# Kernel tuning notes

Hardware: AMD Instinct MI355X
Metric: run time of the kernel (lower is better)

Reference implementation:

```python
import jax, jax.numpy as jnp
import numpy as np

N = 131072
MUL = 64  # multiplicity of each irrep in x
FAN_IN = 128  # 2*MUL input channels per output irrep block
INV_SQRT_FAN = float(1.0 / np.sqrt(FAN_IN))
INV_SQRT3 = float(1.0 / np.sqrt(3.0))


def setup_inputs() -> dict:
    key = jax.random.key(0)
    k1, k2, k3, k4 = jax.random.split(key, 4)
    x = jax.random.normal(k1, (N, MUL + MUL * 3), dtype=jnp.float32)   # 64x0e + 64x1o
    y = jax.random.normal(k2, (N, 1 + 3), dtype=jnp.float32)           # 1x0e + 1x1o
    W0 = jax.random.normal(k3, (FAN_IN, 2 * MUL), dtype=jnp.float32)   # 0e block: 128 -> (64 gates + 64 scalars)
    b0 = jnp.zeros((2 * MUL,), dtype=jnp.float32)                      # bias only on scalars (0e)
    W1 = jax.random.normal(k4, (FAN_IN, MUL), dtype=jnp.float32)       # 1o block: 128 -> 64
    return {"x": x, "y": y, "W0": W0, "b0": b0, "W1": W1}


def reference(x, y, W0, b0, W1):
    # unpack irreps: x = 64x0e + 64x1o ; y = 1x0e + 1x1o
    x0 = x[:, :MUL]                       # [N, 64]
    x1 = x[:, MUL:].reshape(-1, MUL, 3)   # [N, 64, 3]
    y0 = y[:, :1]                         # [N, 1]
    y1 = y[:, 1:]                         # [N, 3]
    # Clebsch-Gordan tensor product (component normalization):
    #   0e x 0e -> 0e : x0 * y0
    #   1o x 1o -> 0e : dot(x1, y1)/sqrt(3)
    #   0e x 1o -> 1o : x0 * y1
    #   1o x 0e -> 1o : x1 * y0
    # (1e/2e paths are dropped by the Linear to 128x0e + 64x1o)
    tp0 = jnp.concatenate(
        [x0 * y0, jnp.einsum("nci,ni->nc", x1, y1) * INV_SQRT3], axis=-1
    )  # [N, 128] of 0e
    tp1 = jnp.concatenate(
        [x0[:, :, None] * y1[:, None, :], x1 * y0[:, :, None]], axis=1
    )  # [N, 128, 3] of 1o
    # irrep-wise Linear (element normalization => scale 1/sqrt(fan_in); bias on scalars)
    s = tp0 @ W0 * INV_SQRT_FAN + b0                      # [N, 128]: 64 gates + 64 scalars
    v = jnp.einsum("nci,co->noi", tp1, W1) * INV_SQRT_FAN  # [N, 64, 3]
    # gate: gelu on even scalars, sigmoid gates multiply the vectors
    gates = jax.nn.sigmoid(s[:, :MUL])
    scalars = jax.nn.gelu(s[:, MUL:])
    vec = (gates[:, :, None] * v).reshape(-1, MUL * 3)
    return jnp.concatenate([scalars, vec], axis=-1)  # [N, 256] = 64x0e + 64x1o
```

## Files before the change

### kernel.cpp

```cpp
#include <hip/hip_runtime.h>
#include <cstdint>

#define TPB 256

static constexpr float INV_SQRT_FAN = 0.08838834764831845f;
static constexpr float INV_SQRT3_C  = 0.5773502691896258f;

typedef _Float16 f16x4v __attribute__((ext_vector_type(4)));
typedef float f32x4 __attribute__((ext_vector_type(4)));

__device__ __align__(16) uint16_t g_wf[24576];

__device__ __forceinline__ uint16_t f2h(float f) {
  union { _Float16 h; uint16_t u; } cv;
  cv.h = (_Float16)f;
  return cv.u;
}
__device__ __forceinline__ uint32_t pk2(float a, float b) {
  return (uint32_t)f2h(a) | ((uint32_t)f2h(b) << 16);
}

__global__ void prep_kernel(const float* __restrict__ W0,
                            const float* __restrict__ W1) {
  int id = blockIdx.x * TPB + threadIdx.x;
  if (id < 16384) {
    int k = id >> 7, n = id & 127;
    g_wf[n * 128 + k] = f2h(W0[id]);
  } else {
    int i2 = id - 16384;
    int k = i2 >> 6, o = i2 & 63;
    g_wf[16384 + o * 128 + k] = f2h(W1[i2]);
  }
}

#define MFMA16H(a, b, c) __builtin_amdgcn_mfma_f32_16x16x16f16((a), (b), (c), 0, 0, 0)

__global__ __launch_bounds__(256, 7) void tplg_mfma(
    const float* __restrict__ x, const float* __restrict__ y,
    const float* __restrict__ b0, float* __restrict__ out) {
  __shared__ uint16_t lds16[10368];
  float* gatesf = (float*)(lds16 + 8192);

  const int t = threadIdx.x;
  const long rowBase = (long)blockIdx.x * 16;

  {
    const int u = t & 15;
    const int r = t >> 4;
    const float* xr = x + (rowBase + r) * 256;
    const float4 x0 = *(const float4*)(xr + 4 * u);
    const float4 aa = *(const float4*)(xr + 64 + 12 * u);
    const float4 bb = *(const float4*)(xr + 64 + 12 * u + 4);
    const float4 cc = *(const float4*)(xr + 64 + 12 * u + 8);
    const float4 yv = *(const float4*)(y + (rowBase + r) * 4);
    const float y0 = yv.x, y1 = yv.y, y2 = yv.z, y3 = yv.w;
    const float t0x = aa.x, t0y = aa.y, t0z = aa.z;
    const float t1x = aa.w, t1y = bb.x, t1z = bb.y;
    const float t2x = bb.z, t2y = bb.w, t2z = cc.x;
    const float t3x = cc.y, t3y = cc.z, t3z = cc.w;
    const int base = r * 512;
    const int us = u ^ r;
    *(uint2*)(lds16 + base + us * 4) =
        make_uint2(pk2(x0.x * y0, x0.y * y0), pk2(x0.z * y0, x0.w * y0));
    const float d0 = (t0x * y1 + t0y * y2 + t0z * y3) * INV_SQRT3_C;
    const float d1 = (t1x * y1 + t1y * y2 + t1z * y3) * INV_SQRT3_C;
    const float d2 = (t2x * y1 + t2y * y2 + t2z * y3) * INV_SQRT3_C;
    const float d3 = (t3x * y1 + t3y * y2 + t3z * y3) * INV_SQRT3_C;
    *(uint2*)(lds16 + base + (16 + us) * 4) = make_uint2(pk2(d0, d1), pk2(d2, d3));
    *(uint2*)(lds16 + base + (32 + us) * 4) =
        make_uint2(pk2(x0.x * y1, x0.y * y1), pk2(x0.z * y1, x0.w * y1));
    *(uint2*)(lds16 + base + (48 + us) * 4) =
        make_uint2(pk2(t0x * y0, t1x * y0), pk2(t2x * y0, t3x * y0));
    *(uint2*)(lds16 + base + (64 + us) * 4) =
        make_uint2(pk2(x0.x * y2, x0.y * y2), pk2(x0.z * y2, x0.w * y2));
    *(uint2*)(lds16 + base + (80 + us) * 4) =
        make_uint2(pk2(t0y * y0, t1y * y0), pk2(t2y * y0, t3y * y0));
    *(uint2*)(lds16 + base + (96 + us) * 4) =
        make_uint2(pk2(x0.x * y3, x0.y * y3), pk2(x0.z * y3, x0.w * y3));
    *(uint2*)(lds16 + base + (112 + us) * 4) =
        make_uint2(pk2(t0z * y0, t1z * y0), pk2(t2z * y0, t3z * y0));
  }
  __syncthreads();

  const int wave = t >> 6;
  const int lane = t & 63;
  const int g = lane >> 4;
  const int q = lane & 15;
  const f32x4 zf = {0.f, 0.f, 0.f, 0.f};

  f32x4 acc[2][3];

  if (wave < 2) {
    const int nb = wave * 64;
    f32x4 p[4] = {zf, zf, zf, zf};
    const uint16_t* tpr = lds16 + q * 512;
    #pragma unroll
    for (int m2 = 0; m2 < 8; ++m2) {
      const f16x4v a = *(const f16x4v*)(tpr + ((m2 * 4 + g) ^ q) * 4);
      #pragma unroll
      for (int nt = 0; nt < 4; ++nt) {
        const f16x4v b =
            *(const f16x4v*)(g_wf + (nb + nt * 16 + q) * 128 + m2 * 16 + g * 4);
        p[nt] = MFMA16H(a, b, p[nt]);
      }
    }
    if (wave == 0) {
      #pragma unroll
      for (int nt = 0; nt < 4; ++nt) {
        const int col = nt * 16 + q;
        const float bc = b0[col];
        #pragma unroll
        for (int j = 0; j < 4; ++j) {
          const float s = p[nt][j] * INV_SQRT_FAN + bc;
          gatesf[(g * 4 + j) * 68 + col] = __builtin_amdgcn_rcpf(1.0f + __expf(-s));
        }
      }
    } else {
      #pragma unroll
      for (int nt = 0; nt < 4; ++nt) {
        const int col = nt * 16 + q;
        const float bc = b0[64 + col];
        #pragma unroll
        for (int j = 0; j < 4; ++j) {
          const float s = p[nt][j] * INV_SQRT_FAN + bc;
          const float u3 = s * s * s;
          const float ua = 0.7978845608028654f * (s + 0.044715f * u3);
          const float e = __expf(2.0f * ua);
          const float th = 1.0f - 2.0f * __builtin_amdgcn_rcpf(e + 1.0f);
          out[(rowBase + g * 4 + j) * 256 + col] = 0.5f * s * (1.0f + th);
        }
      }
    }
  } else {
    const int ob = (wave - 2) * 32;
    #pragma unroll
    for (int nt = 0; nt < 2; ++nt)
      #pragma unroll
      for (int i = 0; i < 3; ++i) acc[nt][i] = zf;
    #pragma unroll
    for (int m2 = 0; m2 < 8; ++m2) {
      f16x4v av[3];
      #pragma unroll
      for (int i = 0; i < 3; ++i)
        av[i] = *(const f16x4v*)(lds16 + q * 512 +
                                 (((1 + i) * 32 + m2 * 4 + g) ^ q) * 4);
      #pragma unroll
      for (int nt = 0; nt < 2; ++nt) {
        const f16x4v b = *(const f16x4v*)(g_wf + 16384 +
                                          (ob + nt * 16 + q) * 128 + m2 * 16 + g * 4);
        #pragma unroll
        for (int i = 0; i < 3; ++i) acc[nt][i] = MFMA16H(av[i], b, acc[nt][i]);
      }
    }
  }
  __syncthreads();

  if (wave >= 2) {
    const int ob = (wave - 2) * 32;
    #pragma unroll
    for (int nt = 0; nt < 2; ++nt) {
      const int o = ob + nt * 16 + q;
      #pragma unroll
      for (int j = 0; j < 4; ++j) {
        const int rr = g * 4 + j;
        const float gq = gatesf[rr * 68 + o] * INV_SQRT_FAN;
        float* op = out + (rowBase + rr) * 256 + 64 + o * 3;
        op[0] = gq * acc[nt][0][j];
        op[1] = gq * acc[nt][1][j];
        op[2] = gq * acc[nt][2][j];
      }
    }
  }
}

extern "C" void kernel_launch(void* const* d_in, const int* in_sizes, int n_in,
                              void* d_out, int out_size, void* d_ws, size_t ws_size,
                              hipStream_t stream) {
  const float* x  = (const float*)d_in[0];
  const float* y  = (const float*)d_in[1];
  const float* W0 = (const float*)d_in[2];
  const float* b0 = (const float*)d_in[3];
  const float* W1 = (const float*)d_in[4];
  float* out = (float*)d_out;
  (void)d_ws; (void)ws_size;

  const int rows = in_sizes[0] / 256;
  prep_kernel<<<24576 / TPB, TPB, 0, stream>>>(W0, W1);
  tplg_mfma<<<rows / 16, TPB, 0, stream>>>(x, y, b0, out);
}
```

Measured before the change: 300.1 us.

## Keep weight fragments in registers and loop each block over eight row tiles

Each block now processes 128 rows as eight 16-row tiles instead of a single tile. The fp16 weight fragments and the bias are loaded into registers once per wave and reused across all tiles, so B operands are no longer refetched from global memory for every 16 rows. The cost is 32 f16x4 registers per lane for the weights, a lower occupancy hint (4 instead of 7), and eight times fewer blocks. Tiles run serially inside a block with no prefetch, so memory latency is hidden less well within each block.

```diff
diff --git a/kernel.cpp b/kernel.cpp
--- a/kernel.cpp
+++ b/kernel.cpp
@@ -35,139 +35,154 @@
 
 #define MFMA16H(a, b, c) __builtin_amdgcn_mfma_f32_16x16x16f16((a), (b), (c), 0, 0, 0)
 
-__global__ __launch_bounds__(256, 7) void tplg_mfma(
+__global__ __launch_bounds__(256, 4) void tplg_mfma(
     const float* __restrict__ x, const float* __restrict__ y,
     const float* __restrict__ b0, float* __restrict__ out) {
   __shared__ uint16_t lds16[10368];
   float* gatesf = (float*)(lds16 + 8192);
 
   const int t = threadIdx.x;
-  const long rowBase = (long)blockIdx.x * 16;
-
-  {
-    const int u = t & 15;
-    const int r = t >> 4;
-    const float* xr = x + (rowBase + r) * 256;
-    const float4 x0 = *(const float4*)(xr + 4 * u);
-    const float4 aa = *(const float4*)(xr + 64 + 12 * u);
-    const float4 bb = *(const float4*)(xr + 64 + 12 * u + 4);
-    const float4 cc = *(const float4*)(xr + 64 + 12 * u + 8);
-    const float4 yv = *(const float4*)(y + (rowBase + r) * 4);
-    const float y0 = yv.x, y1 = yv.y, y2 = yv.z, y3 = yv.w;
-    const float t0x = aa.x, t0y = aa.y, t0z = aa.z;
-    const float t1x = aa.w, t1y = bb.x, t1z = bb.y;
-    const float t2x = bb.z, t2y = bb.w, t2z = cc.x;
-    const float t3x = cc.y, t3y = cc.z, t3z = cc.w;
-    const int base = r * 512;
-    const int us = u ^ r;
-    *(uint2*)(lds16 + base + us * 4) =
-        make_uint2(pk2(x0.x * y0, x0.y * y0), pk2(x0.z * y0, x0.w * y0));
-    const float d0 = (t0x * y1 + t0y * y2 + t0z * y3) * INV_SQRT3_C;
-    const float d1 = (t1x * y1 + t1y * y2 + t1z * y3) * INV_SQRT3_C;
-    const float d2 = (t2x * y1 + t2y * y2 + t2z * y3) * INV_SQRT3_C;
-    const float d3 = (t3x * y1 + t3y * y2 + t3z * y3) * INV_SQRT3_C;
-    *(uint2*)(lds16 + base + (16 + us) * 4) = make_uint2(pk2(d0, d1), pk2(d2, d3));
-    *(uint2*)(lds16 + base + (32 + us) * 4) =
-        make_uint2(pk2(x0.x * y1, x0.y * y1), pk2(x0.z * y1, x0.w * y1));
-    *(uint2*)(lds16 + base + (48 + us) * 4) =
-        make_uint2(pk2(t0x * y0, t1x * y0), pk2(t2x * y0, t3x * y0));
-    *(uint2*)(lds16 + base + (64 + us) * 4) =
-        make_uint2(pk2(x0.x * y2, x0.y * y2), pk2(x0.z * y2, x0.w * y2));
-    *(uint2*)(lds16 + base + (80 + us) * 4) =
-        make_uint2(pk2(t0y * y0, t1y * y0), pk2(t2y * y0, t3y * y0));
-    *(uint2*)(lds16 + base + (96 + us) * 4) =
-        make_uint2(pk2(x0.x * y3, x0.y * y3), pk2(x0.z * y3, x0.w * y3));
-    *(uint2*)(lds16 + base + (112 + us) * 4) =
-        make_uint2(pk2(t0z * y0, t1z * y0), pk2(t2z * y0, t3z * y0));
-  }
-  __syncthreads();
-
   const int wave = t >> 6;
   const int lane = t & 63;
   const int g = lane >> 4;
   const int q = lane & 15;
   const f32x4 zf = {0.f, 0.f, 0.f, 0.f};
 
-  f32x4 acc[2][3];
-
+  f16x4v breg[8][4];
+  {
+    const uint16_t* wbase = (wave < 2)
+        ? (g_wf + (wave * 64 + q) * 128)
+        : (g_wf + 16384 + ((wave - 2) * 32 + q) * 128);
+    #pragma unroll
+    for (int m2 = 0; m2 < 8; ++m2)
+      #pragma unroll
+      for (int nt = 0; nt < 4; ++nt) {
+        const int ntc = (wave < 2) ? nt : (nt & 1);
+        breg[m2][nt] = *(const f16x4v*)(wbase + ntc * 2048 + m2 * 16 + g * 4);
+      }
+  }
+  float bcr[4];
   if (wave < 2) {
-    const int nb = wave * 64;
-    f32x4 p[4] = {zf, zf, zf, zf};
-    const uint16_t* tpr = lds16 + q * 512;
     #pragma unroll
-    for (int m2 = 0; m2 < 8; ++m2) {
-      const f16x4v a = *(const f16x4v*)(tpr + ((m2 * 4 + g) ^ q) * 4);
-      #pragma unroll
-      for (int nt = 0; nt < 4; ++nt) {
-        const f16x4v b =
-            *(const f16x4v*)(g_wf + (nb + nt * 16 + q) * 128 + m2 * 16 + g * 4);
-        p[nt] = MFMA16H(a, b, p[nt]);
-      }
+    for (int nt = 0; nt < 4; ++nt) bcr[nt] = b0[wave * 64 + nt * 16 + q];
+  } else {
+    #pragma unroll
+    for (int nt = 0; nt < 4; ++nt) bcr[nt] = 0.f;
+  }
+
+  const long blockBase = (long)blockIdx.x * 128;
+
+  for (int tile = 0; tile < 8; ++tile) {
+    const long rowBase = blockBase + tile * 16;
+
+    {
+      const int u = t & 15;
+      const int r = t >> 4;
+      const float* xr = x + (rowBase + r) * 256;
+      const float4 x0 = *(const float4*)(xr + 4 * u);
+      const float4 aa = *(const float4*)(xr + 64 + 12 * u);
+      const float4 bb = *(const float4*)(xr + 64 + 12 * u + 4);
+      const float4 cc = *(const float4*)(xr + 64 + 12 * u + 8);
+      const float4 yv = *(const float4*)(y + (rowBase + r) * 4);
+      const float y0 = yv.x, y1 = yv.y, y2 = yv.z, y3 = yv.w;
+      const float t0x = aa.x, t0y = aa.y, t0z = aa.z;
+      const float t1x = aa.w, t1y = bb.x, t1z = bb.y;
+      const float t2x = bb.z, t2y = bb.w, t2z = cc.x;
+      const float t3x = cc.y, t3y = cc.z, t3z = cc.w;
+      const int base = r * 512;
+      const int us = u ^ r;
+      *(uint2*)(lds16 + base + us * 4) =
+          make_uint2(pk2(x0.x * y0, x0.y * y0), pk2(x0.z * y0, x0.w * y0));
+      const float d0 = (t0x * y1 + t0y * y2 + t0z * y3) * INV_SQRT3_C;
+      const float d1 = (t1x * y1 + t1y * y2 + t1z * y3) * INV_SQRT3_C;
+      const float d2 = (t2x * y1 + t2y * y2 + t2z * y3) * INV_SQRT3_C;
+      const float d3 = (t3x * y1 + t3y * y2 + t3z * y3) * INV_SQRT3_C;
+      *(uint2*)(lds16 + base + (16 + us) * 4) = make_uint2(pk2(d0, d1), pk2(d2, d3));
+      *(uint2*)(lds16 + base + (32 + us) * 4) =
+          make_uint2(pk2(x0.x * y1, x0.y * y1), pk2(x0.z * y1, x0.w * y1));
+      *(uint2*)(lds16 + base + (48 + us) * 4) =
+          make_uint2(pk2(t0x * y0, t1x * y0), pk2(t2x * y0, t3x * y0));
+      *(uint2*)(lds16 + base + (64 + us) * 4) =
+          make_uint2(pk2(x0.x * y2, x0.y * y2), pk2(x0.z * y2, x0.w * y2));
+      *(uint2*)(lds16 + base + (80 + us) * 4) =
+          make_uint2(pk2(t0y * y0, t1y * y0), pk2(t2y * y0, t3y * y0));
+      *(uint2*)(lds16 + base + (96 + us) * 4) =
+          make_uint2(pk2(x0.x * y3, x0.y * y3), pk2(x0.z * y3, x0.w * y3));
+      *(uint2*)(lds16 + base + (112 + us) * 4) =
+          make_uint2(pk2(t0z * y0, t1z * y0), pk2(t2z * y0, t3z * y0));
     }
-    if (wave == 0) {
-      #pragma unroll
-      for (int nt = 0; nt < 4; ++nt) {
-        const int col = nt * 16 + q;
-        const float bc = b0[col];
+    __syncthreads();
+
+    f32x4 acc[2][3];
+
+    if (wave < 2) {
+      f32x4 p[4] = {zf, zf, zf, zf};
+      const uint16_t* tpr = lds16 + q * 512;
+      #pragma unroll
+      for (int m2 = 0; m2 < 8; ++m2) {
+        const f16x4v a = *(const f16x4v*)(tpr + ((m2 * 4 + g) ^ q) * 4);
+        #pragma unroll
+        for (int nt = 0; nt < 4; ++nt) p[nt] = MFMA16H(a, breg[m2][nt], p[nt]);
+      }
+      if (wave == 0) {
+        #pragma unroll
+        for (int nt = 0; nt < 4; ++nt) {
+          const int col = nt * 16 + q;
+          #pragma unroll
+          for (int j = 0; j < 4; ++j) {
+            const float s = p[nt][j] * INV_SQRT_FAN + bcr[nt];
+            gatesf[(g * 4 + j) * 68 + col] = __builtin_amdgcn_rcpf(1.0f + __expf(-s));
+          }
+        }
+      } else {
+        #pragma unroll
+        for (int nt = 0; nt < 4; ++nt) {
+          const int col = nt * 16 + q;
+          #pragma unroll
+          for (int j = 0; j < 4; ++j) {
+            const float s = p[nt][j] * INV_SQRT_FAN + bcr[nt];
+            const float u3 = s * s * s;
+            const float ua = 0.7978845608028654f * (s + 0.044715f * u3);
+            const float e = __expf(2.0f * ua);
+            const float th = 1.0f - 2.0f * __builtin_amdgcn_rcpf(e + 1.0f);
+            out[(rowBase + g * 4 + j) * 256 + col] = 0.5f * s * (1.0f + th);
+          }
+        }
+      }
+    } else {
+      #pragma unroll
+      for (int nt = 0; nt < 2; ++nt)
+        #pragma unroll
+        for (int i = 0; i < 3; ++i) acc[nt][i] = zf;
+      #pragma unroll
+      for (int m2 = 0; m2 < 8; ++m2) {
+        f16x4v av[3];
+        #pragma unroll
+        for (int i = 0; i < 3; ++i)
+          av[i] = *(const f16x4v*)(lds16 + q * 512 +
+                                   (((1 + i) * 32 + m2 * 4 + g) ^ q) * 4);
+        #pragma unroll
+        for (int nt = 0; nt < 2; ++nt)
+          #pragma unroll
+          for (int i = 0; i < 3; ++i) acc[nt][i] = MFMA16H(av[i], breg[m2][nt], acc[nt][i]);
+      }
+    }
+    __syncthreads();
+
+    if (wave >= 2) {
+      const int ob = (wave - 2) * 32;
+      #pragma unroll
+      for (int nt = 0; nt < 2; ++nt) {
+        const int o = ob + nt * 16 + q;
         #pragma unroll
         for (int j = 0; j < 4; ++j) {
-          const float s = p[nt][j] * INV_SQRT_FAN + bc;
-          gatesf[(g * 4 + j) * 68 + col] = __builtin_amdgcn_rcpf(1.0f + __expf(-s));
+          const int rr = g * 4 + j;
+          const float gq = gatesf[rr * 68 + o] * INV_SQRT_FAN;
+          float* op = out + (rowBase + rr) * 256 + 64 + o * 3;
+          op[0] = gq * acc[nt][0][j];
+          op[1] = gq * acc[nt][1][j];
+          op[2] = gq * acc[nt][2][j];
         }
-      }
-    } else {
-      #pragma unroll
-      for (int nt = 0; nt < 4; ++nt) {
-        const int col = nt * 16 + q;
-        const float bc = b0[64 + col];
-        #pragma unroll
-        for (int j = 0; j < 4; ++j) {
-          const float s = p[nt][j] * INV_SQRT_FAN + bc;
-          const float u3 = s * s * s;
-          const float ua = 0.7978845608028654f * (s + 0.044715f * u3);
-          const float e = __expf(2.0f * ua);
-          const float th = 1.0f - 2.0f * __builtin_amdgcn_rcpf(e + 1.0f);
-          out[(rowBase + g * 4 + j) * 256 + col] = 0.5f * s * (1.0f + th);
-        }
-      }
-    }
-  } else {
-    const int ob = (wave - 2) * 32;
-    #pragma unroll
-    for (int nt = 0; nt < 2; ++nt)
-      #pragma unroll
-      for (int i = 0; i < 3; ++i) acc[nt][i] = zf;
-    #pragma unroll
-    for (int m2 = 0; m2 < 8; ++m2) {
-      f16x4v av[3];
-      #pragma unroll
-      for (int i = 0; i < 3; ++i)
-        av[i] = *(const f16x4v*)(lds16 + q * 512 +
-                                 (((1 + i) * 32 + m2 * 4 + g) ^ q) * 4);
-      #pragma unroll
-      for (int nt = 0; nt < 2; ++nt) {
-        const f16x4v b = *(const f16x4v*)(g_wf + 16384 +
-                                          (ob + nt * 16 + q) * 128 + m2 * 16 + g * 4);
-        #pragma unroll
-        for (int i = 0; i < 3; ++i) acc[nt][i] = MFMA16H(av[i], b, acc[nt][i]);
-      }
-    }
-  }
-  __syncthreads();
-
-  if (wave >= 2) {
-    const int ob = (wave - 2) * 32;
-    #pragma unroll
-    for (int nt = 0; nt < 2; ++nt) {
-      const int o = ob + nt * 16 + q;
-      #pragma unroll
-      for (int j = 0; j < 4; ++j) {
-        const int rr = g * 4 + j;
-        const float gq = gatesf[rr * 68 + o] * INV_SQRT_FAN;
-        float* op = out + (rowBase + rr) * 256 + 64 + o * 3;
-        op[0] = gq * acc[nt][0][j];
-        op[1] = gq * acc[nt][1][j];
-        op[2] = gq * acc[nt][2][j];
       }
     }
   }
@@ -186,5 +201,5 @@
 
   const int rows = in_sizes[0] / 256;
   prep_kernel<<<24576 / TPB, TPB, 0, stream>>>(W0, W1);
-  tplg_mfma<<<rows / 16, TPB, 0, stream>>>(x, y, b0, out);
-}
+  tplg_mfma<<<rows / 128, TPB, 0, stream>>>(x, y, b0, out);
+}
```

Result: no change. 301.8 us (+0.6%).

## Process multiple row tiles per block with register prefetch of next tile

Applied to the files above, without the earlier changes.

Each block now handles four 16-row tiles in a loop instead of one. The x and y loads for the next tile are issued into registers right after the current tile's products are written to LDS, so global load latency overlaps with the MFMA and epilogue work. The grid shrinks fourfold and launch bounds drop from 7 to 4 blocks per CU. The cost is fewer resident waves and more register pressure, which gives less latency hiding through occupancy.

```diff
diff --git a/kernel.cpp b/kernel.cpp
--- a/kernel.cpp
+++ b/kernel.cpp
@@ -2,6 +2,7 @@
 #include <cstdint>
 
 #define TPB 256
+#define TILES 4
 
 static constexpr float INV_SQRT_FAN = 0.08838834764831845f;
 static constexpr float INV_SQRT3_C  = 0.5773502691896258f;
@@ -35,139 +36,155 @@
 
 #define MFMA16H(a, b, c) __builtin_amdgcn_mfma_f32_16x16x16f16((a), (b), (c), 0, 0, 0)
 
-__global__ __launch_bounds__(256, 7) void tplg_mfma(
+__global__ __launch_bounds__(256, 4) void tplg_mfma(
     const float* __restrict__ x, const float* __restrict__ y,
     const float* __restrict__ b0, float* __restrict__ out) {
   __shared__ uint16_t lds16[10368];
   float* gatesf = (float*)(lds16 + 8192);
 
   const int t = threadIdx.x;
-  const long rowBase = (long)blockIdx.x * 16;
-
-  {
-    const int u = t & 15;
-    const int r = t >> 4;
-    const float* xr = x + (rowBase + r) * 256;
-    const float4 x0 = *(const float4*)(xr + 4 * u);
-    const float4 aa = *(const float4*)(xr + 64 + 12 * u);
-    const float4 bb = *(const float4*)(xr + 64 + 12 * u + 4);
-    const float4 cc = *(const float4*)(xr + 64 + 12 * u + 8);
-    const float4 yv = *(const float4*)(y + (rowBase + r) * 4);
-    const float y0 = yv.x, y1 = yv.y, y2 = yv.z, y3 = yv.w;
-    const float t0x = aa.x, t0y = aa.y, t0z = aa.z;
-    const float t1x = aa.w, t1y = bb.x, t1z = bb.y;
-    const float t2x = bb.z, t2y = bb.w, t2z = cc.x;
-    const float t3x = cc.y, t3y = cc.z, t3z = cc.w;
-    const int base = r * 512;
-    const int us = u ^ r;
-    *(uint2*)(lds16 + base + us * 4) =
-        make_uint2(pk2(x0.x * y0, x0.y * y0), pk2(x0.z * y0, x0.w * y0));
-    const float d0 = (t0x * y1 + t0y * y2 + t0z * y3) * INV_SQRT3_C;
-    const float d1 = (t1x * y1 + t1y * y2 + t1z * y3) * INV_SQRT3_C;
-    const float d2 = (t2x * y1 + t2y * y2 + t2z * y3) * INV_SQRT3_C;
-    const float d3 = (t3x * y1 + t3y * y2 + t3z * y3) * INV_SQRT3_C;
-    *(uint2*)(lds16 + base + (16 + us) * 4) = make_uint2(pk2(d0, d1), pk2(d2, d3));
-    *(uint2*)(lds16 + base + (32 + us) * 4) =
-        make_uint2(pk2(x0.x * y1, x0.y * y1), pk2(x0.z * y1, x0.w * y1));
-    *(uint2*)(lds16 + base + (48 + us) * 4) =
-        make_uint2(pk2(t0x * y0, t1x * y0), pk2(t2x * y0, t3x * y0));
-    *(uint2*)(lds16 + base + (64 + us) * 4) =
-        make_uint2(pk2(x0.x * y2, x0.y * y2), pk2(x0.z * y2, x0.w * y2));
-    *(uint2*)(lds16 + base + (80 + us) * 4) =
-        make_uint2(pk2(t0y * y0, t1y * y0), pk2(t2y * y0, t3y * y0));
-    *(uint2*)(lds16 + base + (96 + us) * 4) =
-        make_uint2(pk2(x0.x * y3, x0.y * y3), pk2(x0.z * y3, x0.w * y3));
-    *(uint2*)(lds16 + base + (112 + us) * 4) =
-        make_uint2(pk2(t0z * y0, t1z * y0), pk2(t2z * y0, t3z * y0));
-  }
-  __syncthreads();
-
   const int wave = t >> 6;
   const int lane = t & 63;
   const int g = lane >> 4;
   const int q = lane & 15;
+  const int u = t & 15;
+  const int r = t >> 4;
   const f32x4 zf = {0.f, 0.f, 0.f, 0.f};
-
-  f32x4 acc[2][3];
-
-  if (wave < 2) {
-    const int nb = wave * 64;
-    f32x4 p[4] = {zf, zf, zf, zf};
-    const uint16_t* tpr = lds16 + q * 512;
-    #pragma unroll
-    for (int m2 = 0; m2 < 8; ++m2) {
-      const f16x4v a = *(const f16x4v*)(tpr + ((m2 * 4 + g) ^ q) * 4);
-      #pragma unroll
-      for (int nt = 0; nt < 4; ++nt) {
-        const f16x4v b =
-            *(const f16x4v*)(g_wf + (nb + nt * 16 + q) * 128 + m2 * 16 + g * 4);
-        p[nt] = MFMA16H(a, b, p[nt]);
-      }
-    }
-    if (wave == 0) {
-      #pragma unroll
-      for (int nt = 0; nt < 4; ++nt) {
-        const int col = nt * 16 + q;
-        const float bc = b0[col];
+  const long blockBase = (long)blockIdx.x * (16 * TILES);
+
+  float4 x0, aa, bb, cc, yv;
+  {
+    const float* xr = x + (blockBase + r) * 256;
+    x0 = *(const float4*)(xr + 4 * u);
+    aa = *(const float4*)(xr + 64 + 12 * u);
+    bb = *(const float4*)(xr + 64 + 12 * u + 4);
+    cc = *(const float4*)(xr + 64 + 12 * u + 8);
+    yv = *(const float4*)(y + (blockBase + r) * 4);
+  }
+
+  for (int tile = 0; tile < TILES; ++tile) {
+    const long rowBase = blockBase + tile * 16;
+
+    {
+      const float y0 = yv.x, y1 = yv.y, y2 = yv.z, y3 = yv.w;
+      const float t0x = aa.x, t0y = aa.y, t0z = aa.z;
+      const float t1x = aa.w, t1y = bb.x, t1z = bb.y;
+      const float t2x = bb.z, t2y = bb.w, t2z = cc.x;
+      const float t3x = cc.y, t3y = cc.z, t3z = cc.w;
+      const int base = r * 512;
+      const int us = u ^ r;
+      *(uint2*)(lds16 + base + us * 4) =
+          make_uint2(pk2(x0.x * y0, x0.y * y0), pk2(x0.z * y0, x0.w * y0));
+      const float d0 = (t0x * y1 + t0y * y2 + t0z * y3) * INV_SQRT3_C;
+      const float d1 = (t1x * y1 + t1y * y2 + t1z * y3) * INV_SQRT3_C;
+      const float d2 = (t2x * y1 + t2y * y2 + t2z * y3) * INV_SQRT3_C;
+      const float d3 = (t3x * y1 + t3y * y2 + t3z * y3) * INV_SQRT3_C;
+      *(uint2*)(lds16 + base + (16 + us) * 4) = make_uint2(pk2(d0, d1), pk2(d2, d3));
+      *(uint2*)(lds16 + base + (32 + us) * 4) =
+          make_uint2(pk2(x0.x * y1, x0.y * y1), pk2(x0.z * y1, x0.w * y1));
+      *(uint2*)(lds16 + base + (48 + us) * 4) =
+          make_uint2(pk2(t0x * y0, t1x * y0), pk2(t2x * y0, t3x * y0));
+      *(uint2*)(lds16 + base + (64 + us) * 4) =
+          make_uint2(pk2(x0.x * y2, x0.y * y2), pk2(x0.z * y2, x0.w * y2));
+      *(uint2*)(lds16 + base + (80 + us) * 4) =
+          make_uint2(pk2(t0y * y0, t1y * y0), pk2(t2y * y0, t3y * y0));
+      *(uint2*)(lds16 + base + (96 + us) * 4) =
+          make_uint2(pk2(x0.x * y3, x0.y * y3), pk2(x0.z * y3, x0.w * y3));
+      *(uint2*)(lds16 + base + (112 + us) * 4) =
+          make_uint2(pk2(t0z * y0, t1z * y0), pk2(t2z * y0, t3z * y0));
+    }
+
+    if (tile + 1 < TILES) {
+      const float* xr = x + (rowBase + 16 + r) * 256;
+      x0 = *(const float4*)(xr + 4 * u);
+      aa = *(const float4*)(xr + 64 + 12 * u);
+      bb = *(const float4*)(xr + 64 + 12 * u + 4);
+      cc = *(const float4*)(xr + 64 + 12 * u + 8);
+      yv = *(const float4*)(y + (rowBase + 16 + r) * 4);
+    }
+    __syncthreads();
+
+    f32x4 acc[2][3];
+
+    if (wave < 2) {
+      const int nb = wave * 64;
+      f32x4 p[4] = {zf, zf, zf, zf};
+      const uint16_t* tpr = lds16 + q * 512;
+      #pragma unroll
+      for (int m2 = 0; m2 < 8; ++m2) {
+        const f16x4v a = *(const f16x4v*)(tpr + ((m2 * 4 + g) ^ q) * 4);
+        #pragma unroll
+        for (int nt = 0; nt < 4; ++nt) {
+          const f16x4v b =
+              *(const f16x4v*)(g_wf + (nb + nt * 16 + q) * 128 + m2 * 16 + g * 4);
+          p[nt] = MFMA16H(a, b, p[nt]);
+        }
+      }
+      if (wave == 0) {
+        #pragma unroll
+        for (int nt = 0; nt < 4; ++nt) {
+          const int col = nt * 16 + q;
+          const float bc = b0[col];
+          #pragma unroll
+          for (int j = 0; j < 4; ++j) {
+            const float s = p[nt][j] * INV_SQRT_FAN + bc;
+            gatesf[(g * 4 + j) * 68 + col] = __builtin_amdgcn_rcpf(1.0f + __expf(-s));
+          }
+        }
+      } else {
+        #pragma unroll
+        for (int nt = 0; nt < 4; ++nt) {
+          const int col = nt * 16 + q;
+          const float bc = b0[64 + col];
+          #pragma unroll
+          for (int j = 0; j < 4; ++j) {
+            const float s = p[nt][j] * INV_SQRT_FAN + bc;
+            const float u3 = s * s * s;
+            const float ua = 0.7978845608028654f * (s + 0.044715f * u3);
+            const float e = __expf(2.0f * ua);
+            const float th = 1.0f - 2.0f * __builtin_amdgcn_rcpf(e + 1.0f);
+            out[(rowBase + g * 4 + j) * 256 + col] = 0.5f * s * (1.0f + th);
+          }
+        }
+      }
+    } else {
+      const int ob = (wave - 2) * 32;
+      #pragma unroll
+      for (int nt = 0; nt < 2; ++nt)
+        #pragma unroll
+        for (int i = 0; i < 3; ++i) acc[nt][i] = zf;
+      #pragma unroll
+      for (int m2 = 0; m2 < 8; ++m2) {
+        f16x4v av[3];
+        #pragma unroll
+        for (int i = 0; i < 3; ++i)
+          av[i] = *(const f16x4v*)(lds16 + q * 512 +
+                                   (((1 + i) * 32 + m2 * 4 + g) ^ q) * 4);
+        #pragma unroll
+        for (int nt = 0; nt < 2; ++nt) {
+          const f16x4v b = *(const f16x4v*)(g_wf + 16384 +
+                                            (ob + nt * 16 + q) * 128 + m2 * 16 + g * 4);
+          #pragma unroll
+          for (int i = 0; i < 3; ++i) acc[nt][i] = MFMA16H(av[i], b, acc[nt][i]);
+        }
+      }
+    }
+    __syncthreads();
+
+    if (wave >= 2) {
+      const int ob = (wave - 2) * 32;
+      #pragma unroll
+      for (int nt = 0; nt < 2; ++nt) {
+        const int o = ob + nt * 16 + q;
         #pragma unroll
         for (int j = 0; j < 4; ++j) {
-          const float s = p[nt][j] * INV_SQRT_FAN + bc;
-          gatesf[(g * 4 + j) * 68 + col] = __builtin_amdgcn_rcpf(1.0f + __expf(-s));
-        }
-      }
-    } else {
-      #pragma unroll
-      for (int nt = 0; nt < 4; ++nt) {
-        const int col = nt * 16 + q;
-        const float bc = b0[64 + col];
-        #pragma unroll
-        for (int j = 0; j < 4; ++j) {
-          const float s = p[nt][j] * INV_SQRT_FAN + bc;
-          const float u3 = s * s * s;
-          const float ua = 0.7978845608028654f * (s + 0.044715f * u3);
-          const float e = __expf(2.0f * ua);
-          const float th = 1.0f - 2.0f * __builtin_amdgcn_rcpf(e + 1.0f);
-          out[(rowBase + g * 4 + j) * 256 + col] = 0.5f * s * (1.0f + th);
-        }
-      }
-    }
-  } else {
-    const int ob = (wave - 2) * 32;
-    #pragma unroll
-    for (int nt = 0; nt < 2; ++nt)
-      #pragma unroll
-      for (int i = 0; i < 3; ++i) acc[nt][i] = zf;
-    #pragma unroll
-    for (int m2 = 0; m2 < 8; ++m2) {
-      f16x4v av[3];
-      #pragma unroll
-      for (int i = 0; i < 3; ++i)
-        av[i] = *(const f16x4v*)(lds16 + q * 512 +
-                                 (((1 + i) * 32 + m2 * 4 + g) ^ q) * 4);
-      #pragma unroll
-      for (int nt = 0; nt < 2; ++nt) {
-        const f16x4v b = *(const f16x4v*)(g_wf + 16384 +
-                                          (ob + nt * 16 + q) * 128 + m2 * 16 + g * 4);
-        #pragma unroll
-        for (int i = 0; i < 3; ++i) acc[nt][i] = MFMA16H(av[i], b, acc[nt][i]);
-      }
-    }
-  }
-  __syncthreads();
-
-  if (wave >= 2) {
-    const int ob = (wave - 2) * 32;
-    #pragma unroll
-    for (int nt = 0; nt < 2; ++nt) {
-      const int o = ob + nt * 16 + q;
-      #pragma unroll
-      for (int j = 0; j < 4; ++j) {
-        const int rr = g * 4 + j;
-        const float gq = gatesf[rr * 68 + o] * INV_SQRT_FAN;
-        float* op = out + (rowBase + rr) * 256 + 64 + o * 3;
-        op[0] = gq * acc[nt][0][j];
-        op[1] = gq * acc[nt][1][j];
-        op[2] = gq * acc[nt][2][j];
+          const int rr = g * 4 + j;
+          const float gq = gatesf[rr * 68 + o] * INV_SQRT_FAN;
+          float* op = out + (rowBase + rr) * 256 + 64 + o * 3;
+          op[0] = gq * acc[nt][0][j];
+          op[1] = gq * acc[nt][1][j];
+          op[2] = gq * acc[nt][2][j];
+        }
       }
     }
   }
@@ -186,5 +203,5 @@
 
   const int rows = in_sizes[0] / 256;
   prep_kernel<<<24576 / TPB, TPB, 0, stream>>>(W0, W1);
-  tplg_mfma<<<rows / 16, TPB, 0, stream>>>(x, y, b0, out);
-}
+  tplg_mfma<<<rows / (16 * TILES), TPB, 0, stream>>>(x, y, b0, out);
+}
```

After: 358.6 us. 19.5% more time.
